# Performance work log

Hardware: AMD Instinct MI355X
Metric: run time of the kernel (lower is better)

## Reference

```python
import jax, jax.numpy as jnp
import numpy as np

V, E, H, B, P, Q = 100000, 300, 256, 64, 400, 50
NEG = -1e7


def _gru_param(k, s=0.08):
    k1, k2, k3, k4 = jax.random.split(k, 4)
    return (jax.random.normal(k1, (2, 3 * H, E)) * s,
            jax.random.normal(k2, (2, 3 * H, H)) * s,
            jax.random.normal(k3, (2, 3 * H)) * s,
            jax.random.normal(k4, (2, 3 * H)) * s)


def setup_inputs() -> dict:
    key = jax.random.key(0)
    ks = jax.random.split(key, 10)
    emb = (jax.random.normal(ks[0], (V, E)) * 0.1).at[0].set(0.0)  # padding_idx=0 row zeroed
    passage = jax.random.randint(ks[1], (B, P), 1, V)
    question = jax.random.randint(ks[2], (B, Q), 1, V)
    # variable lengths, padding (token 0) at the tail like pack_padded_sequence assumes
    p_len = 200 + (jnp.arange(B) * 7) % (P - 200)
    q_len = 20 + (jnp.arange(B) * 3) % (Q - 20)
    passage = jnp.where(jnp.arange(P)[None, :] < p_len[:, None], passage, 0)
    question = jnp.where(jnp.arange(Q)[None, :] < q_len[:, None], question, 0)
    pW_ih, pW_hh, pb_ih, pb_hh = _gru_param(ks[3])
    qW_ih, qW_hh, qb_ih, qb_hh = _gru_param(ks[4])
    start_w = jax.random.normal(ks[5], (6 * H,)) * 0.05
    start_b = jax.random.normal(ks[6], ()) * 0.05
    end_w = jax.random.normal(ks[7], (6 * H,)) * 0.05
    end_b = jax.random.normal(ks[8], ()) * 0.05
    return dict(passage=passage, question=question, emb=emb,
                pW_ih=pW_ih, pW_hh=pW_hh, pb_ih=pb_ih, pb_hh=pb_hh,
                qW_ih=qW_ih, qW_hh=qW_hh, qb_ih=qb_ih, qb_hh=qb_hh,
                start_w=start_w, start_b=start_b, end_w=end_w, end_b=end_b)


def bi_gru(x, mask, Wih, Whh, bih, bhh):
    """Bidirectional GRU with packed-sequence-equivalent masking.
    x: (B,T,E), mask: (B,T) float. Returns (B,T,2H). Padded outputs are 0,
    and the backward pass starts at the true last token (mask freezes state)."""
    m = mask[..., None]                                          # (B,T,1)
    xproj = jnp.einsum('bte,dhe->dbth', x, Wih) + bih[:, None, None, :]  # (2,B,T,3H)

    def run(xp, mm, Whh_d, bhh_d):
        def step(h, inp):
            xt, mt = inp                                         # (B,3H),(B,1)
            hp = h @ Whh_d.T + bhh_d
            r = jax.nn.sigmoid(xt[:, :H] + hp[:, :H])
            z = jax.nn.sigmoid(xt[:, H:2 * H] + hp[:, H:2 * H])
            n = jnp.tanh(xt[:, 2 * H:] + r * hp[:, 2 * H:])
            h_new = (1 - z) * n + z * h
            h_new = mt * h_new + (1 - mt) * h
            return h_new, h_new * mt
        h0 = jnp.zeros((xp.shape[0], H), xp.dtype)
        _, out = jax.lax.scan(step, h0, (xp.transpose(1, 0, 2), mm.transpose(1, 0, 2)))
        return out.transpose(1, 0, 2)                            # (B,T,H)

    fwd = run(xproj[0], m, Whh[0], bhh[0])
    bwd = run(xproj[1][:, ::-1], m[:, ::-1], Whh[1], bhh[1])[:, ::-1]
    return jnp.concatenate([fwd, bwd], axis=-1)


def reference(passage, question, emb,
              pW_ih, pW_hh, pb_ih, pb_hh,
              qW_ih, qW_hh, qb_ih, qb_hh,
              start_w, start_b, end_w, end_b):
    p_mask = (passage != 0).astype(jnp.float32)                  # (B,P)
    q_mask = (question != 0).astype(jnp.float32)                 # (B,Q)
    Hp = bi_gru(emb[passage], p_mask, pW_ih, pW_hh, pb_ih, pb_hh)  # (B,P,2H)
    Hq = bi_gru(emb[question], q_mask, qW_ih, qW_hh, qb_ih, qb_hh)  # (B,Q,2H)

    # Trilinear attention: decompose Linear over the cat([p, q, p*q]) terms
    w1, w2, w3 = start_w[:2 * H], start_w[2 * H:4 * H], start_w[4 * H:]
    scores = (Hp @ w1)[:, :, None] + (Hq @ w2)[:, None, :] \
        + jnp.einsum('bpd,bqd->bpq', Hp * w3, Hq) + start_b      # (B,P,Q)

    # allennlp masked_softmax: softmax(vector*mask) * mask, renormalized
    a = jax.nn.softmax(scores * q_mask[:, None, :], axis=-1) * q_mask[:, None, :]
    a = a / (a.sum(axis=-1, keepdims=True) + 1e-13)

    wavg = jnp.einsum('bpq,bqd->bpd', a, Hq)                     # (B,P,2H)
    combined = jnp.concatenate([Hp, wavg, Hp * wavg], axis=-1)   # (B,P,6H)

    start_logits = jnp.where(p_mask > 0, combined @ start_w + start_b, NEG)
    end_logits = jnp.where(p_mask > 0, combined @ end_w + end_b, NEG)
    log_mask = jnp.log(p_mask + 1e-45)
    softmax_start = jax.nn.log_softmax(start_logits + log_mask, axis=-1)
    softmax_end = jax.nn.log_softmax(end_logits + log_mask, axis=-1)
    return start_logits, end_logits, softmax_start, softmax_end
```

## Files before the change

### kernel.cpp

```cpp
#include <hip/hip_runtime.h>
#include <math.h>

constexpr int Bb = 64;
constexpr int Pp = 400;
constexpr int Qq = 50;
constexpr int Ee = 300;
constexpr int Hh = 256;
constexpr int H3 = 768;
constexpr int Dd = 512;

#define NEGC (-10000000.0f)
#define LOGTINY (-103.278929903f)

typedef _Float16 h2 __attribute__((ext_vector_type(2)));
typedef _Float16 f16x8 __attribute__((ext_vector_type(8)));
typedef float f32x4 __attribute__((ext_vector_type(4)));

__device__ __forceinline__ float allred(float v){
  #pragma unroll
  for (int off = 1; off < 64; off <<= 1) v += __shfl_xor(v, off);
  return v;
}
__device__ __forceinline__ float allmax(float v){
  #pragma unroll
  for (int off = 1; off < 64; off <<= 1) v = fmaxf(v, __shfl_xor(v, off));
  return v;
}
__device__ __forceinline__ float sigm(float x){ return 1.f / (1.f + expf(-x)); }

__device__ __forceinline__ float dot2f(unsigned a, unsigned b, float c){
#if __has_builtin(__builtin_amdgcn_fdot2)
  return __builtin_amdgcn_fdot2(__builtin_bit_cast(h2, a), __builtin_bit_cast(h2, b), c, false);
#else
  float r = c;
  asm("v_dot2_f32_f16 %0, %1, %2, %0" : "+v"(r) : "v"(a), "v"(b));
  return r;
#endif
}

__global__ __launch_bounds__(256) void prep_w16(const float* __restrict__ pW,
                                                const float* __restrict__ qW,
                                                unsigned* __restrict__ w16){
  int idx = blockIdx.x * 256 + threadIdx.x;
  if (idx >= 2 * 2 * 3 * 16 * 512 * 4) return;
  int c = idx & 3;
  int t = (idx >> 2) & 511;
  int q = (idx >> 11) & 15;
  int gg = idx >> 15;
  int gate = gg % 3, gd = gg / 3;
  int d = gd & 1, g = gd >> 1;
  int j = t & 255, half = t >> 8;
  int p = half * 64 + q * 4 + c;
  int row = gate * 256 + j;
  const float* W = g ? qW : pW;
  const float* src = W + ((size_t)d * H3 + row) * Hh + 2 * p;
  _Float16 a = (_Float16)src[0], b = (_Float16)src[1];
  unsigned short ua, ub;
  __builtin_memcpy(&ua, &a, 2); __builtin_memcpy(&ub, &b, 2);
  w16[idx] = (unsigned)ua | ((unsigned)ub << 16);
}

__global__ __launch_bounds__(512) void xproj_mfma(const int* __restrict__ tok,
                                                  const float* __restrict__ emb,
                                                  const float* __restrict__ Wih,
                                                  const float* __restrict__ bih,
                                                  float* __restrict__ xp, int T){
  __shared__ __align__(16) _Float16 As[128][72];
  __shared__ __align__(16) _Float16 Bs[128][72];
  int tid = threadIdx.x;
  int m0 = blockIdx.y * 128;
  int nt = blockIdx.x;
  int d = nt / 6, h0 = (nt % 6) * 128;
  int wid = tid >> 6, lane = tid & 63;
  int wr = wid >> 2, wc = wid & 3;

  int srow = tid >> 2;
  int scol = (tid & 3) * 16;
  const float* aRow = emb + (size_t)tok[m0 + srow] * Ee;
  const float* bRow = Wih + ((size_t)d * H3 + h0 + srow) * Ee;

  f32x4 acc[4][2] = {};

  for (int k0 = 0; k0 < 320; k0 += 64){
    #pragma unroll
    for (int half = 0; half < 2; ++half){
      int k = k0 + scol + half * 8;
      float4 va0, va1, vb0, vb1;
      if (k + 8 <= Ee){
        va0 = *(const float4*)(aRow + k); va1 = *(const float4*)(aRow + k + 4);
        vb0 = *(const float4*)(bRow + k); vb1 = *(const float4*)(bRow + k + 4);
      } else if (k + 4 <= Ee){
        va0 = *(const float4*)(aRow + k); va1 = make_float4(0.f, 0.f, 0.f, 0.f);
        vb0 = *(const float4*)(bRow + k); vb1 = make_float4(0.f, 0.f, 0.f, 0.f);
      } else {
        va0 = va1 = vb0 = vb1 = make_float4(0.f, 0.f, 0.f, 0.f);
      }
      f16x8 a8 = { (_Float16)va0.x, (_Float16)va0.y, (_Float16)va0.z, (_Float16)va0.w,
                   (_Float16)va1.x, (_Float16)va1.y, (_Float16)va1.z, (_Float16)va1.w };
      f16x8 b8 = { (_Float16)vb0.x, (_Float16)vb0.y, (_Float16)vb0.z, (_Float16)vb0.w,
                   (_Float16)vb1.x, (_Float16)vb1.y, (_Float16)vb1.z, (_Float16)vb1.w };
      *(f16x8*)&As[srow][scol + half * 8] = a8;
      *(f16x8*)&Bs[srow][scol + half * 8] = b8;
    }
    __syncthreads();
    #pragma unroll
    for (int kc = 0; kc < 2; ++kc){
      int kb = kc * 32 + (lane >> 4) * 8;
      f16x8 af[4], bf[2];
      #pragma unroll
      for (int i = 0; i < 4; ++i) af[i] = *(const f16x8*)&As[wr * 64 + i * 16 + (lane & 15)][kb];
      #pragma unroll
      for (int jn = 0; jn < 2; ++jn) bf[jn] = *(const f16x8*)&Bs[wc * 32 + jn * 16 + (lane & 15)][kb];
      #pragma unroll
      for (int i = 0; i < 4; ++i)
        #pragma unroll
        for (int jn = 0; jn < 2; ++jn)
          acc[i][jn] = __builtin_amdgcn_mfma_f32_16x16x32_f16(af[i], bf[jn], acc[i][jn], 0, 0, 0);
    }
    __syncthreads();
  }

  #pragma unroll
  for (int jn = 0; jn < 2; ++jn){
    int h = h0 + wc * 32 + jn * 16 + (lane & 15);
    float bv = bih[d * H3 + h];
    #pragma unroll
    for (int i = 0; i < 4; ++i){
      #pragma unroll
      for (int r = 0; r < 4; ++r){
        int m = m0 + wr * 64 + i * 16 + (lane >> 4) * 4 + r;
        int bI = m / T, tI = m - bI * T;
        xp[(((size_t)d * Bb + bI) * T + tI) * H3 + h] = acc[i][jn][r] + bv;
      }
    }
  }
}

__global__ __launch_bounds__(512) __attribute__((amdgpu_waves_per_eu(2, 2)))
void gru_kernel(const int* __restrict__ ptok,
                const int* __restrict__ qtok,
                const float* __restrict__ xpp,
                const float* __restrict__ xpq,
                const unsigned* __restrict__ w16,
                const float* __restrict__ pbhh,
                const float* __restrict__ qbhh,
                float* __restrict__ Hp,
                float* __restrict__ Hq){
  int wg = blockIdx.x;
  bool isp = wg < 128;
  int lw = isp ? wg : wg - 128;
  int d = lw & 1, b = lw >> 1;
  int T = isp ? Pp : Qq;
  const int* tok = (isp ? ptok : qtok) + b * T;
  const float* xrow = (isp ? xpp : xpq) + ((size_t)d * Bb + b) * T * H3;
  int gd = (isp ? 0 : 2) + d;
  const float* bhh = (isp ? pbhh : qbhh) + d * H3;
  float* Hout = (isp ? Hp : Hq) + (size_t)b * T * Dd + d * Hh;

  __shared__ unsigned hbuf[2][128];
  __shared__ float pa[Hh], pb[Hh], pn[Hh];

  int t = threadIdx.x;
  int j = t & 255, half = t >> 8, lane = t & 63;

  unsigned w0[64], w1[64], w2[64];
  {
    const uint4* wq = (const uint4*)w16 + (size_t)gd * 3 * 16 * 512;
    #pragma unroll
    for (int q = 0; q < 16; ++q){
      uint4 v0 = wq[(0 * 16 + q) * 512 + t];
      uint4 v1 = wq[(1 * 16 + q) * 512 + t];
      uint4 v2 = wq[(2 * 16 + q) * 512 + t];
      w0[4 * q + 0] = v0.x; w0[4 * q + 1] = v0.y; w0[4 * q + 2] = v0.z; w0[4 * q + 3] = v0.w;
      w1[4 * q + 0] = v1.x; w1[4 * q + 1] = v1.y; w1[4 * q + 2] = v1.z; w1[4 * q + 3] = v1.w;
      w2[4 * q + 0] = v2.x; w2[4 * q + 1] = v2.y; w2[4 * q + 2] = v2.z; w2[4 * q + 3] = v2.w;
    }
  }
  #pragma unroll
  for (int i = 0; i < 64; ++i){
    asm volatile("" : "+v"(w0[i]));
    asm volatile("" : "+v"(w1[i]));
    asm volatile("" : "+v"(w2[i]));
  }

  float bh0 = bhh[j], bh1 = bhh[Hh + j], bh2 = bhh[2 * Hh + j];
  float h_old = 0.f;
  if (t < 128) hbuf[1][t] = 0u;
  __syncthreads();

  int t0 = d ? (T - 1) : 0;
  float pre0 = 0.f, pre1 = 0.f, pre2 = 0.f;
  if (half == 0){
    pre0 = xrow[(size_t)t0 * H3 + j];
    pre1 = xrow[(size_t)t0 * H3 + Hh + j];
    pre2 = xrow[(size_t)t0 * H3 + 2 * Hh + j];
  }

  for (int s = 0; s < T; ++s){
    int tt = d ? (T - 1 - s) : s;
    unsigned vh = hbuf[(s + 1) & 1][half * 64 + lane];
    float a0 = 0.f, a1 = 0.f, a2 = 0.f;
    #pragma unroll
    for (int p = 0; p < 64; ++p){
      unsigned hv = (unsigned)__builtin_amdgcn_readlane((int)vh, p);
      a0 = dot2f(w0[p], hv, a0);
      a1 = dot2f(w1[p], hv, a1);
      a2 = dot2f(w2[p], hv, a2);
    }
    if (half == 1){ pa[j] = a0; pb[j] = a1; pn[j] = a2; }
    __syncthreads();
    if (half == 0){
      float xt0 = pre0, xt1 = pre1, xt2 = pre2;
      if (s + 1 < T){
        int tn = d ? (T - 2 - s) : (s + 1);
        pre0 = xrow[(size_t)tn * H3 + j];
        pre1 = xrow[(size_t)tn * H3 + Hh + j];
        pre2 = xrow[(size_t)tn * H3 + 2 * Hh + j];
      }
      float g0 = a0 + pa[j] + bh0;
      float g1 = a1 + pb[j] + bh1;
      float g2 = a2 + pn[j] + bh2;
      float r = sigm(xt0 + g0);
      float z = sigm(xt1 + g1);
      float n = tanhf(xt2 + r * g2);
      float hnew = (1.f - z) * n + z * h_old;
      float m = (tok[tt] != 0) ? 1.f : 0.f;
      float hm = m * hnew + (1.f - m) * h_old;
      h_old = hm;
      ((_Float16*)hbuf[s & 1])[j] = (_Float16)hm;
      Hout[(size_t)tt * Dd + j] = hm * m;
    }
    __syncthreads();
  }
}

__global__ __launch_bounds__(512) void attn_kernel(const float* __restrict__ Hp,
                                                   const float* __restrict__ Hq,
                                                   const int* __restrict__ ptok,
                                                   const int* __restrict__ qtok,
                                                   const float* __restrict__ start_w,
                                                   const float* __restrict__ sbp,
                                                   const float* __restrict__ end_w,
                                                   const float* __restrict__ ebp,
                                                   float* __restrict__ out){
  extern __shared__ __align__(16) float lds[];
  float* hqs = lds;
  float* s2s = hqs + Qq * Dd;
  float* qms = s2s + 64;
  float* scw = qms + 64;
  float* aw  = scw + 512;

  int b = blockIdx.y, pc = blockIdx.x;
  int tid = threadIdx.x, wid = tid >> 6, lane = tid & 63;
  float sb = sbp[0], eb = ebp[0];

  float w1r[8], w2r[8], w3r[8], e1r[8], e2r[8], e3r[8];
  #pragma unroll
  for (int i = 0; i < 8; ++i){
    int c = lane * 8 + i;
    w1r[i] = start_w[c]; w2r[i] = start_w[Dd + c]; w3r[i] = start_w[2 * Dd + c];
    e1r[i] = end_w[c];   e2r[i] = end_w[Dd + c];   e3r[i] = end_w[2 * Dd + c];
  }
  for (int idx = tid; idx < Qq * Dd; idx += 512) hqs[idx] = Hq[(size_t)b * Qq * Dd + idx];
  __syncthreads();

  for (int q = wid; q < Qq; q += 8){
    float part = 0.f;
    const float* hq = hqs + q * Dd + lane * 8;
    #pragma unroll
    for (int i = 0; i < 8; ++i) part += hq[i] * w2r[i];
    part = allred(part);
    if (lane == 0){
      s2s[q] = part;
      qms[q] = (qtok[b * Qq + q] != 0) ? 1.f : 0.f;
    }
  }
  __syncthreads();

  for (int p = pc * 100 + wid; p < pc * 100 + 100; p += 8){
    const float* hprow = Hp + ((size_t)b * Pp + p) * Dd + lane * 8;
    float4 hv0 = *(const float4*)hprow;
    float4 hv1 = *(const float4*)(hprow + 4);
    float hpc[8] = {hv0.x, hv0.y, hv0.z, hv0.w, hv1.x, hv1.y, hv1.z, hv1.w};
    float hw3[8], he3[8];
    float s1 = 0.f, ed = 0.f;
    #pragma unroll
    for (int i = 0; i < 8; ++i){
      hw3[i] = hpc[i] * w3r[i];
      he3[i] = hpc[i] * e3r[i];
      s1 += hpc[i] * w1r[i];
      ed += hpc[i] * e1r[i];
    }
    #pragma unroll
    for (int off = 1; off < 64; off <<= 1){
      s1 += __shfl_xor(s1, off);
      ed += __shfl_xor(ed, off);
    }
    for (int q = 0; q < Qq; ++q){
      const float4* hq4 = (const float4*)(hqs + q * Dd + lane * 8);
      float4 a0 = hq4[0], a1 = hq4[1];
      float dot = hw3[0] * a0.x + hw3[1] * a0.y + hw3[2] * a0.z + hw3[3] * a0.w
                + hw3[4] * a1.x + hw3[5] * a1.y + hw3[6] * a1.z + hw3[7] * a1.w;
      dot = allred(dot);
      if (lane == 0) scw[wid * 64 + q] = (s1 + s2s[q] + dot + sb) * qms[q];
    }
    float v = (lane < Qq) ? scw[wid * 64 + lane] : -1e30f;
    float M = allmax(v);
    float ev = (lane < Qq) ? expf(v - M) : 0.f;
    float S = allred(ev);
    float am = (lane < Qq) ? (ev / S) * qms[lane] : 0.f;
    float Sm = allred(am);
    float af = am / (Sm + 1e-13f);
    if (lane < Qq) aw[wid * 64 + lane] = af;
    float wv[8] = {0.f, 0.f, 0.f, 0.f, 0.f, 0.f, 0.f, 0.f};
    for (int q = 0; q < Qq; ++q){
      float aq = aw[wid * 64 + q];
      const float4* hq4 = (const float4*)(hqs + q * Dd + lane * 8);
      float4 a0 = hq4[0], a1 = hq4[1];
      wv[0] += aq * a0.x; wv[1] += aq * a0.y; wv[2] += aq * a0.z; wv[3] += aq * a0.w;
      wv[4] += aq * a1.x; wv[5] += aq * a1.y; wv[6] += aq * a1.z; wv[7] += aq * a1.w;
    }
    float acc2 = 0.f, acc3 = 0.f, acc4 = 0.f, acc5 = 0.f;
    #pragma unroll
    for (int i = 0; i < 8; ++i){
      acc2 += wv[i] * w2r[i];
      acc3 += hw3[i] * wv[i];
      acc4 += wv[i] * e2r[i];
      acc5 += he3[i] * wv[i];
    }
    #pragma unroll
    for (int off = 1; off < 64; off <<= 1){
      acc2 += __shfl_xor(acc2, off);
      acc3 += __shfl_xor(acc3, off);
      acc4 += __shfl_xor(acc4, off);
      acc5 += __shfl_xor(acc5, off);
    }
    if (lane == 0){
      bool pm = (ptok[b * Pp + p] != 0);
      out[(size_t)b * Pp + p]                   = pm ? (s1 + acc2 + acc3 + sb) : NEGC;
      out[(size_t)Bb * Pp + (size_t)b * Pp + p] = pm ? (ed + acc4 + acc5 + eb) : NEGC;
    }
  }
}

__global__ __launch_bounds__(512) void lsm_kernel(const int* __restrict__ ptok,
                                                  float* __restrict__ out){
  int b = blockIdx.x >> 1, sel = blockIdx.x & 1;
  const float* lg = out + (size_t)sel * Bb * Pp + (size_t)b * Pp;
  float* o = out + (size_t)(2 + sel) * Bb * Pp + (size_t)b * Pp;
  int tid = threadIdx.x;
  __shared__ float red1[8];
  __shared__ float red2[8];
  float x = -1e30f;
  if (tid < Pp) x = lg[tid] + ((ptok[b * Pp + tid] != 0) ? 0.f : LOGTINY);
  float m = allmax(x);
  if ((tid & 63) == 0) red1[tid >> 6] = m;
  __syncthreads();
  float M = red1[0];
  #pragma unroll
  for (int i = 1; i < 8; ++i) M = fmaxf(M, red1[i]);
  float e = (tid < Pp) ? expf(x - M) : 0.f;
  float s = allred(e);
  if ((tid & 63) == 0) red2[tid >> 6] = s;
  __syncthreads();
  float S = 0.f;
  #pragma unroll
  for (int i = 0; i < 8; ++i) S += red2[i];
  if (tid < Pp) o[tid] = (x - M) - logf(S);
}

extern "C" void kernel_launch(void* const* d_in, const int* in_sizes, int n_in,
                              void* d_out, int out_size, void* d_ws, size_t ws_size,
                              hipStream_t stream){
  const int*   passage  = (const int*)d_in[0];
  const int*   question = (const int*)d_in[1];
  const float* emb      = (const float*)d_in[2];
  const float* pW_ih    = (const float*)d_in[3];
  const float* pW_hh    = (const float*)d_in[4];
  const float* pb_ih    = (const float*)d_in[5];
  const float* pb_hh    = (const float*)d_in[6];
  const float* qW_ih    = (const float*)d_in[7];
  const float* qW_hh    = (const float*)d_in[8];
  const float* qb_ih    = (const float*)d_in[9];
  const float* qb_hh    = (const float*)d_in[10];
  const float* start_w  = (const float*)d_in[11];
  const float* start_b  = (const float*)d_in[12];
  const float* end_w    = (const float*)d_in[13];
  const float* end_b    = (const float*)d_in[14];
  float* out = (float*)d_out;

  float*    ws  = (float*)d_ws;
  unsigned* w16 = (unsigned*)ws;
  float*    xpp = ws + 393216;
  float*    xpq = ws + 39714816;
  float*    Hp  = ws + 44630016;
  float*    Hq  = ws + 57737216;

  hipLaunchKernelGGL(prep_w16, dim3(1536), dim3(256), 0, stream, pW_hh, qW_hh, w16);
  hipLaunchKernelGGL(xproj_mfma, dim3(12, 200), dim3(512), 0, stream,
                     passage, emb, pW_ih, pb_ih, xpp, Pp);
  hipLaunchKernelGGL(xproj_mfma, dim3(12, 25), dim3(512), 0, stream,
                     question, emb, qW_ih, qb_ih, xpq, Qq);
  hipLaunchKernelGGL(gru_kernel, dim3(256), dim3(512), 0, stream,
                     passage, question, xpp, xpq, w16, pb_hh, qb_hh, Hp, Hq);
  size_t attn_lds = (size_t)(Qq * Dd + 64 + 64 + 512 + 512) * sizeof(float);
  hipLaunchKernelGGL(attn_kernel, dim3(4, 64), dim3(512), attn_lds, stream,
                     Hp, Hq, passage, question, start_w, start_b, end_w, end_b, out);
  hipLaunchKernelGGL(lsm_kernel, dim3(128), dim3(512), 0, stream, passage, out);
}
```

Baseline: 0.9999 ms.

## Split GRU recurrent matvec across four thread quarters with 1024-thread blocks

The recurrent GRU kernel now uses 1024 threads per block, so each of four quarters handles 64 of the 256 hidden inputs instead of two halves handling 128. Each thread keeps half as many fp16 weight registers and runs half as many dot2 steps per timestep, which shortens the serial critical path of each step. In exchange, three partial sums per gate go through LDS and are reduced by quarter 0, and 1024-thread blocks with 4 waves/EU add synchronisation cost. The weight pre-pack kernel's layout is changed to match.

```diff
diff --git a/kernel.cpp b/kernel.cpp
--- a/kernel.cpp
+++ b/kernel.cpp
@@ -42,15 +42,15 @@
                                                 const float* __restrict__ qW,
                                                 unsigned* __restrict__ w16){
   int idx = blockIdx.x * 256 + threadIdx.x;
-  if (idx >= 2 * 2 * 3 * 16 * 512 * 4) return;
+  if (idx >= 2 * 2 * 3 * 8 * 1024 * 4) return;
   int c = idx & 3;
-  int t = (idx >> 2) & 511;
-  int q = (idx >> 11) & 15;
+  int t = (idx >> 2) & 1023;
+  int ql = (idx >> 12) & 7;
   int gg = idx >> 15;
   int gate = gg % 3, gd = gg / 3;
   int d = gd & 1, g = gd >> 1;
-  int j = t & 255, half = t >> 8;
-  int p = half * 64 + q * 4 + c;
+  int j = t & 255, qq = t >> 8;
+  int p = qq * 32 + ql * 4 + c;
   int row = gate * 256 + j;
   const float* W = g ? qW : pW;
   const float* src = W + ((size_t)d * H3 + row) * Hh + 2 * p;
@@ -136,7 +136,7 @@
   }
 }
 
-__global__ __launch_bounds__(512) __attribute__((amdgpu_waves_per_eu(2, 2)))
+__global__ __attribute__((amdgpu_flat_work_group_size(1024, 1024), amdgpu_waves_per_eu(4, 4)))
 void gru_kernel(const int* __restrict__ ptok,
                 const int* __restrict__ qtok,
                 const float* __restrict__ xpp,
@@ -158,58 +158,62 @@
   float* Hout = (isp ? Hp : Hq) + (size_t)b * T * Dd + d * Hh;
 
   __shared__ unsigned hbuf[2][128];
-  __shared__ float pa[Hh], pb[Hh], pn[Hh];
+  __shared__ float part[3][3][Hh];
 
   int t = threadIdx.x;
-  int j = t & 255, half = t >> 8, lane = t & 63;
-
-  unsigned w0[64], w1[64], w2[64];
+  int j = t & 255, qq = t >> 8, lane = t & 63;
+
+  unsigned w0[32], w1[32], w2[32];
   {
-    const uint4* wq = (const uint4*)w16 + (size_t)gd * 3 * 16 * 512;
-    #pragma unroll
-    for (int q = 0; q < 16; ++q){
-      uint4 v0 = wq[(0 * 16 + q) * 512 + t];
-      uint4 v1 = wq[(1 * 16 + q) * 512 + t];
-      uint4 v2 = wq[(2 * 16 + q) * 512 + t];
-      w0[4 * q + 0] = v0.x; w0[4 * q + 1] = v0.y; w0[4 * q + 2] = v0.z; w0[4 * q + 3] = v0.w;
-      w1[4 * q + 0] = v1.x; w1[4 * q + 1] = v1.y; w1[4 * q + 2] = v1.z; w1[4 * q + 3] = v1.w;
-      w2[4 * q + 0] = v2.x; w2[4 * q + 1] = v2.y; w2[4 * q + 2] = v2.z; w2[4 * q + 3] = v2.w;
-    }
-  }
-  #pragma unroll
-  for (int i = 0; i < 64; ++i){
+    const uint4* wq = (const uint4*)w16;
+    #pragma unroll
+    for (int ql = 0; ql < 8; ++ql){
+      uint4 v0 = wq[(((size_t)gd * 3 + 0) * 8 + ql) * 1024 + t];
+      uint4 v1 = wq[(((size_t)gd * 3 + 1) * 8 + ql) * 1024 + t];
+      uint4 v2 = wq[(((size_t)gd * 3 + 2) * 8 + ql) * 1024 + t];
+      w0[4 * ql + 0] = v0.x; w0[4 * ql + 1] = v0.y; w0[4 * ql + 2] = v0.z; w0[4 * ql + 3] = v0.w;
+      w1[4 * ql + 0] = v1.x; w1[4 * ql + 1] = v1.y; w1[4 * ql + 2] = v1.z; w1[4 * ql + 3] = v1.w;
+      w2[4 * ql + 0] = v2.x; w2[4 * ql + 1] = v2.y; w2[4 * ql + 2] = v2.z; w2[4 * ql + 3] = v2.w;
+    }
+  }
+  #pragma unroll
+  for (int i = 0; i < 32; ++i){
     asm volatile("" : "+v"(w0[i]));
     asm volatile("" : "+v"(w1[i]));
     asm volatile("" : "+v"(w2[i]));
   }
 
-  float bh0 = bhh[j], bh1 = bhh[Hh + j], bh2 = bhh[2 * Hh + j];
+  float bh0 = 0.f, bh1 = 0.f, bh2 = 0.f;
   float h_old = 0.f;
-  if (t < 128) hbuf[1][t] = 0u;
-  __syncthreads();
-
+  float pre0 = 0.f, pre1 = 0.f, pre2 = 0.f;
   int t0 = d ? (T - 1) : 0;
-  float pre0 = 0.f, pre1 = 0.f, pre2 = 0.f;
-  if (half == 0){
+  if (qq == 0){
+    bh0 = bhh[j]; bh1 = bhh[Hh + j]; bh2 = bhh[2 * Hh + j];
     pre0 = xrow[(size_t)t0 * H3 + j];
     pre1 = xrow[(size_t)t0 * H3 + Hh + j];
     pre2 = xrow[(size_t)t0 * H3 + 2 * Hh + j];
-  }
+    if (j < 128) hbuf[1][j] = 0u;
+  }
+  __syncthreads();
 
   for (int s = 0; s < T; ++s){
     int tt = d ? (T - 1 - s) : s;
-    unsigned vh = hbuf[(s + 1) & 1][half * 64 + lane];
+    unsigned vh = hbuf[(s + 1) & 1][qq * 32 + (lane & 31)];
     float a0 = 0.f, a1 = 0.f, a2 = 0.f;
     #pragma unroll
-    for (int p = 0; p < 64; ++p){
+    for (int p = 0; p < 32; ++p){
       unsigned hv = (unsigned)__builtin_amdgcn_readlane((int)vh, p);
       a0 = dot2f(w0[p], hv, a0);
       a1 = dot2f(w1[p], hv, a1);
       a2 = dot2f(w2[p], hv, a2);
     }
-    if (half == 1){ pa[j] = a0; pb[j] = a1; pn[j] = a2; }
+    if (qq != 0){
+      part[qq - 1][0][j] = a0;
+      part[qq - 1][1][j] = a1;
+      part[qq - 1][2][j] = a2;
+    }
     __syncthreads();
-    if (half == 0){
+    if (qq == 0){
       float xt0 = pre0, xt1 = pre1, xt2 = pre2;
       if (s + 1 < T){
         int tn = d ? (T - 2 - s) : (s + 1);
@@ -217,9 +221,9 @@
         pre1 = xrow[(size_t)tn * H3 + Hh + j];
         pre2 = xrow[(size_t)tn * H3 + 2 * Hh + j];
       }
-      float g0 = a0 + pa[j] + bh0;
-      float g1 = a1 + pb[j] + bh1;
-      float g2 = a2 + pn[j] + bh2;
+      float g0 = a0 + part[0][0][j] + part[1][0][j] + part[2][0][j] + bh0;
+      float g1 = a1 + part[0][1][j] + part[1][1][j] + part[2][1][j] + bh1;
+      float g2 = a2 + part[0][2][j] + part[1][2][j] + part[2][2][j] + bh2;
       float r = sigm(xt0 + g0);
       float z = sigm(xt1 + g1);
       float n = tanhf(xt2 + r * g2);
@@ -401,7 +405,7 @@
                      passage, emb, pW_ih, pb_ih, xpp, Pp);
   hipLaunchKernelGGL(xproj_mfma, dim3(12, 25), dim3(512), 0, stream,
                      question, emb, qW_ih, qb_ih, xpq, Qq);
-  hipLaunchKernelGGL(gru_kernel, dim3(256), dim3(512), 0, stream,
+  hipLaunchKernelGGL(gru_kernel, dim3(256), dim3(1024), 0, stream,
                      passage, question, xpp, xpq, w16, pb_hh, qb_hh, Hp, Hq);
   size_t attn_lds = (size_t)(Qq * Dd + 64 + 64 + 512 + 512) * sizeof(float);
   hipLaunchKernelGGL(attn_kernel, dim3(4, 64), dim3(512), attn_lds, stream,
```

Result: no change. 1.004 ms (+0.4%).

## Split GRU recurrent weights across registers, LDS and streamed global loads; store xproj in fp16

Applied to the files above, without the earlier changes.

The recurrent weights were previously held entirely in registers, with occupancy pinned at 2 waves per EU. They are now split three ways: a quarter stays in registers, about 37% is staged in LDS, and the rest is re-read from global/L2 on every timestep. prep_w16 writes the weights in a matching split layout. The input projections xpp/xpq are stored as fp16, which halves that traffic. This frees registers and cuts xproj bandwidth, at the cost of per-step LDS and global weight loads on the latency-critical recurrence and some precision loss on the projections.

```diff
diff --git a/kernel.cpp b/kernel.cpp
--- a/kernel.cpp
+++ b/kernel.cpp
@@ -37,6 +37,8 @@
   return r;
 #endif
 }
+
+#define U4C(v,c) ((c)==0?(v).x:((c)==1?(v).y:((c)==2?(v).z:(v).w)))
 
 __global__ __launch_bounds__(256) void prep_w16(const float* __restrict__ pW,
                                                 const float* __restrict__ qW,
@@ -57,14 +59,20 @@
   _Float16 a = (_Float16)src[0], b = (_Float16)src[1];
   unsigned short ua, ub;
   __builtin_memcpy(&ua, &a, 2); __builtin_memcpy(&ub, &b, 2);
-  w16[idx] = (unsigned)ua | ((unsigned)ub << 16);
+  unsigned val = (unsigned)ua | ((unsigned)ub << 16);
+
+  size_t u4idx;
+  if (q < 4)       u4idx = ((size_t)gg * 4 + q) * 512 + t;
+  else if (q < 10) u4idx = 24576 + ((size_t)gg * 6 + (q - 4)) * 512 + t;
+  else             u4idx = 61440 + ((size_t)gg * 6 + (q - 10)) * 512 + t;
+  w16[u4idx * 4 + c] = val;
 }
 
 __global__ __launch_bounds__(512) void xproj_mfma(const int* __restrict__ tok,
                                                   const float* __restrict__ emb,
                                                   const float* __restrict__ Wih,
                                                   const float* __restrict__ bih,
-                                                  float* __restrict__ xp, int T){
+                                                  _Float16* __restrict__ xp, int T){
   __shared__ __align__(16) _Float16 As[128][72];
   __shared__ __align__(16) _Float16 Bs[128][72];
   int tid = threadIdx.x;
@@ -130,17 +138,17 @@
       for (int r = 0; r < 4; ++r){
         int m = m0 + wr * 64 + i * 16 + (lane >> 4) * 4 + r;
         int bI = m / T, tI = m - bI * T;
-        xp[(((size_t)d * Bb + bI) * T + tI) * H3 + h] = acc[i][jn][r] + bv;
+        xp[(((size_t)d * Bb + bI) * T + tI) * H3 + h] = (_Float16)(acc[i][jn][r] + bv);
       }
     }
   }
 }
 
-__global__ __launch_bounds__(512) __attribute__((amdgpu_waves_per_eu(2, 2)))
+__global__ __launch_bounds__(512)
 void gru_kernel(const int* __restrict__ ptok,
                 const int* __restrict__ qtok,
-                const float* __restrict__ xpp,
-                const float* __restrict__ xpq,
+                const _Float16* __restrict__ xpp,
+                const _Float16* __restrict__ xpq,
                 const unsigned* __restrict__ w16,
                 const float* __restrict__ pbhh,
                 const float* __restrict__ qbhh,
@@ -152,36 +160,39 @@
   int d = lw & 1, b = lw >> 1;
   int T = isp ? Pp : Qq;
   const int* tok = (isp ? ptok : qtok) + b * T;
-  const float* xrow = (isp ? xpp : xpq) + ((size_t)d * Bb + b) * T * H3;
+  const _Float16* xrow = (isp ? xpp : xpq) + ((size_t)d * Bb + b) * T * H3;
   int gd = (isp ? 0 : 2) + d;
   const float* bhh = (isp ? pbhh : qbhh) + d * H3;
   float* Hout = (isp ? Hp : Hq) + (size_t)b * T * Dd + d * Hh;
 
+  __shared__ __align__(16) uint4 ldsW[18 * 512];
   __shared__ unsigned hbuf[2][128];
   __shared__ float pa[Hh], pb[Hh], pn[Hh];
 
   int t = threadIdx.x;
   int j = t & 255, half = t >> 8, lane = t & 63;
 
-  unsigned w0[64], w1[64], w2[64];
-  {
-    const uint4* wq = (const uint4*)w16 + (size_t)gd * 3 * 16 * 512;
-    #pragma unroll
-    for (int q = 0; q < 16; ++q){
-      uint4 v0 = wq[(0 * 16 + q) * 512 + t];
-      uint4 v1 = wq[(1 * 16 + q) * 512 + t];
-      uint4 v2 = wq[(2 * 16 + q) * 512 + t];
-      w0[4 * q + 0] = v0.x; w0[4 * q + 1] = v0.y; w0[4 * q + 2] = v0.z; w0[4 * q + 3] = v0.w;
-      w1[4 * q + 0] = v1.x; w1[4 * q + 1] = v1.y; w1[4 * q + 2] = v1.z; w1[4 * q + 3] = v1.w;
-      w2[4 * q + 0] = v2.x; w2[4 * q + 1] = v2.y; w2[4 * q + 2] = v2.z; w2[4 * q + 3] = v2.w;
-    }
-  }
-  #pragma unroll
-  for (int i = 0; i < 64; ++i){
-    asm volatile("" : "+v"(w0[i]));
-    asm volatile("" : "+v"(w1[i]));
-    asm volatile("" : "+v"(w2[i]));
-  }
+  const uint4* wR = (const uint4*)w16 + (size_t)(gd * 3) * 4 * 512;
+  unsigned wr0[16], wr1[16], wr2[16];
+  #pragma unroll
+  for (int q = 0; q < 4; ++q){
+    uint4 v0 = wR[(0 * 4 + q) * 512 + t];
+    uint4 v1 = wR[(1 * 4 + q) * 512 + t];
+    uint4 v2 = wR[(2 * 4 + q) * 512 + t];
+    wr0[4 * q + 0] = v0.x; wr0[4 * q + 1] = v0.y; wr0[4 * q + 2] = v0.z; wr0[4 * q + 3] = v0.w;
+    wr1[4 * q + 0] = v1.x; wr1[4 * q + 1] = v1.y; wr1[4 * q + 2] = v1.z; wr1[4 * q + 3] = v1.w;
+    wr2[4 * q + 0] = v2.x; wr2[4 * q + 1] = v2.y; wr2[4 * q + 2] = v2.z; wr2[4 * q + 3] = v2.w;
+  }
+  #pragma unroll
+  for (int i = 0; i < 16; ++i){
+    asm volatile("" : "+v"(wr0[i]));
+    asm volatile("" : "+v"(wr1[i]));
+    asm volatile("" : "+v"(wr2[i]));
+  }
+  const uint4* wL = (const uint4*)w16 + 24576 + (size_t)(gd * 3) * 6 * 512;
+  #pragma unroll
+  for (int u = 0; u < 18; ++u) ldsW[u * 512 + t] = wL[u * 512 + t];
+  const uint4* wS = (const uint4*)w16 + 61440 + (size_t)(gd * 3) * 6 * 512;
 
   float bh0 = bhh[j], bh1 = bhh[Hh + j], bh2 = bhh[2 * Hh + j];
   float h_old = 0.f;
@@ -191,31 +202,68 @@
   int t0 = d ? (T - 1) : 0;
   float pre0 = 0.f, pre1 = 0.f, pre2 = 0.f;
   if (half == 0){
-    pre0 = xrow[(size_t)t0 * H3 + j];
-    pre1 = xrow[(size_t)t0 * H3 + Hh + j];
-    pre2 = xrow[(size_t)t0 * H3 + 2 * Hh + j];
+    pre0 = (float)xrow[(size_t)t0 * H3 + j];
+    pre1 = (float)xrow[(size_t)t0 * H3 + Hh + j];
+    pre2 = (float)xrow[(size_t)t0 * H3 + 2 * Hh + j];
   }
 
   for (int s = 0; s < T; ++s){
     int tt = d ? (T - 1 - s) : s;
     unsigned vh = hbuf[(s + 1) & 1][half * 64 + lane];
     float a0 = 0.f, a1 = 0.f, a2 = 0.f;
-    #pragma unroll
-    for (int p = 0; p < 64; ++p){
-      unsigned hv = (unsigned)__builtin_amdgcn_readlane((int)vh, p);
-      a0 = dot2f(w0[p], hv, a0);
-      a1 = dot2f(w1[p], hv, a1);
-      a2 = dot2f(w2[p], hv, a2);
-    }
+
+    uint4 sA0 = wS[0 * 512 + t], sA1 = wS[1 * 512 + t], sA2 = wS[2 * 512 + t],
+          sA3 = wS[3 * 512 + t], sA4 = wS[4 * 512 + t], sA5 = wS[5 * 512 + t];
+
+    #pragma unroll
+    for (int q = 0; q < 4; ++q)
+      #pragma unroll
+      for (int c = 0; c < 4; ++c){
+        unsigned hv = (unsigned)__builtin_amdgcn_readlane((int)vh, q * 4 + c);
+        a0 = dot2f(wr0[4 * q + c], hv, a0);
+        a1 = dot2f(wr1[4 * q + c], hv, a1);
+        a2 = dot2f(wr2[4 * q + c], hv, a2);
+      }
+
+    #pragma unroll
+    for (int qb = 0; qb < 6; ++qb){
+      uint4 l0 = ldsW[(0 * 6 + qb) * 512 + t];
+      uint4 l1 = ldsW[(1 * 6 + qb) * 512 + t];
+      uint4 l2 = ldsW[(2 * 6 + qb) * 512 + t];
+      #pragma unroll
+      for (int c = 0; c < 4; ++c){
+        unsigned hv = (unsigned)__builtin_amdgcn_readlane((int)vh, 16 + qb * 4 + c);
+        a0 = dot2f(U4C(l0, c), hv, a0);
+        a1 = dot2f(U4C(l1, c), hv, a1);
+        a2 = dot2f(U4C(l2, c), hv, a2);
+      }
+    }
+
+    #define CONS(v, qi, ACC) { _Pragma("unroll") \
+      for (int c = 0; c < 4; ++c){ \
+        unsigned hv = (unsigned)__builtin_amdgcn_readlane((int)vh, 40 + (qi) * 4 + c); \
+        ACC = dot2f(U4C(v, c), hv, ACC); } }
+    uint4 sB0 = wS[6 * 512 + t],  sB1 = wS[7 * 512 + t],  sB2 = wS[8 * 512 + t],
+          sB3 = wS[9 * 512 + t],  sB4 = wS[10 * 512 + t], sB5 = wS[11 * 512 + t];
+    CONS(sA0, 0, a0) CONS(sA1, 1, a0) CONS(sA2, 2, a0)
+    CONS(sA3, 3, a0) CONS(sA4, 4, a0) CONS(sA5, 5, a0)
+    uint4 sC0 = wS[12 * 512 + t], sC1 = wS[13 * 512 + t], sC2 = wS[14 * 512 + t],
+          sC3 = wS[15 * 512 + t], sC4 = wS[16 * 512 + t], sC5 = wS[17 * 512 + t];
+    CONS(sB0, 0, a1) CONS(sB1, 1, a1) CONS(sB2, 2, a1)
+    CONS(sB3, 3, a1) CONS(sB4, 4, a1) CONS(sB5, 5, a1)
+    CONS(sC0, 0, a2) CONS(sC1, 1, a2) CONS(sC2, 2, a2)
+    CONS(sC3, 3, a2) CONS(sC4, 4, a2) CONS(sC5, 5, a2)
+    #undef CONS
+
     if (half == 1){ pa[j] = a0; pb[j] = a1; pn[j] = a2; }
     __syncthreads();
     if (half == 0){
       float xt0 = pre0, xt1 = pre1, xt2 = pre2;
       if (s + 1 < T){
         int tn = d ? (T - 2 - s) : (s + 1);
-        pre0 = xrow[(size_t)tn * H3 + j];
-        pre1 = xrow[(size_t)tn * H3 + Hh + j];
-        pre2 = xrow[(size_t)tn * H3 + 2 * Hh + j];
+        pre0 = (float)xrow[(size_t)tn * H3 + j];
+        pre1 = (float)xrow[(size_t)tn * H3 + Hh + j];
+        pre2 = (float)xrow[(size_t)tn * H3 + 2 * Hh + j];
       }
       float g0 = a0 + pa[j] + bh0;
       float g1 = a1 + pb[j] + bh1;
@@ -389,12 +437,12 @@
   const float* end_b    = (const float*)d_in[14];
   float* out = (float*)d_out;
 
-  float*    ws  = (float*)d_ws;
-  unsigned* w16 = (unsigned*)ws;
-  float*    xpp = ws + 393216;
-  float*    xpq = ws + 39714816;
-  float*    Hp  = ws + 44630016;
-  float*    Hq  = ws + 57737216;
+  float*     ws  = (float*)d_ws;
+  unsigned*  w16 = (unsigned*)ws;
+  _Float16*  xpp = (_Float16*)(ws + 393216);
+  _Float16*  xpq = (_Float16*)(ws + 20054016);
+  float*     Hp  = ws + 22511616;
+  float*     Hq  = ws + 35618816;
 
   hipLaunchKernelGGL(prep_w16, dim3(1536), dim3(256), 0, stream, pW_hh, qW_hh, w16);
   hipLaunchKernelGGL(xproj_mfma, dim3(12, 200), dim3(512), 0, stream,
```

After: 972.8 us. 1.03x faster.
